# Kernel tuning notes

Hardware: AMD Instinct MI355X
Metric: run time of the kernel (lower is better)

## Reference

```python
import jax, jax.numpy as jnp
import numpy as np

N_NODE = 100000
N_EDGE = 800000
IN_DIM = 128
OUT_DIM = 128
ATTN_DIM = 64
N_REL = 200
N_ENT = 40000
BATCH = 64
N_RELA_ROWS = 2 * N_REL + 1  # 401


def setup_inputs() -> dict:
    key = jax.random.key(0)
    ks = jax.random.split(key, 16)
    # edges: [E, 6] -> col0: r_idx (batch idx), col2: rel, col4: sub, col5: obj
    r_idx = jax.random.randint(ks[0], (N_EDGE,), 0, BATCH)
    rel = jax.random.randint(ks[1], (N_EDGE,), 0, N_RELA_ROWS)
    sub = jax.random.randint(ks[2], (N_EDGE,), 0, N_NODE)
    obj = jax.random.randint(ks[3], (N_EDGE,), 0, N_NODE)
    zeros_col = jnp.zeros((N_EDGE,), dtype=jnp.int32)
    edges = jnp.stack([r_idx, zeros_col, rel, zeros_col, sub, obj], axis=1)

    hidden = jax.random.normal(ks[4], (N_NODE, IN_DIM), dtype=jnp.float32)
    q_sub = jax.random.randint(ks[5], (BATCH,), 0, N_ENT)
    q_rel = jax.random.randint(ks[6], (BATCH,), 0, N_RELA_ROWS)
    nodes = jnp.stack([
        jax.random.randint(ks[7], (N_NODE,), 0, BATCH),
        jax.random.randint(ks[8], (N_NODE,), 0, N_ENT)], axis=1)
    old_nodes_new_idx = jax.random.randint(ks[9], (50000,), 0, N_NODE)

    s = 0.05
    rela_embed = jax.random.normal(ks[10], (N_RELA_ROWS, IN_DIM), dtype=jnp.float32) * s
    Ws = jax.random.normal(ks[11], (IN_DIM, ATTN_DIM), dtype=jnp.float32) * s
    Wr = jax.random.normal(ks[12], (IN_DIM, ATTN_DIM), dtype=jnp.float32) * s
    Wqr = jax.random.normal(ks[13], (IN_DIM, ATTN_DIM), dtype=jnp.float32) * s
    bqr = jnp.zeros((ATTN_DIM,), dtype=jnp.float32)
    wa = jax.random.normal(ks[14], (ATTN_DIM, 1), dtype=jnp.float32) * s
    ba = jnp.zeros((1,), dtype=jnp.float32)
    W_h = jax.random.normal(ks[15], (IN_DIM, OUT_DIM), dtype=jnp.float32) * s

    return {"q_sub": q_sub, "q_rel": q_rel, "hidden": hidden, "edges": edges,
            "nodes": nodes, "old_nodes_new_idx": old_nodes_new_idx, "batchsize": BATCH,
            "rela_embed": rela_embed, "Ws": Ws, "Wr": Wr, "Wqr": Wqr, "bqr": bqr,
            "wa": wa, "ba": ba, "W_h": W_h}


def reference(q_sub, q_rel, hidden, edges, nodes, old_nodes_new_idx, batchsize,
              rela_embed, Ws, Wr, Wqr, bqr, wa, ba, W_h):
    sub = edges[:, 4]
    rel = edges[:, 2]
    obj = edges[:, 5]
    r_idx = edges[:, 0]
    n_node = nodes.shape[0]

    hs = hidden[sub]                    # [E, in_dim]  gather
    hr = rela_embed[rel]                # [E, in_dim]
    h_qr = rela_embed[q_rel][r_idx]     # [E, in_dim]

    # MESS_FUNC == 'TransE'
    message = hs + hr

    # attention MLP: sigmoid(w_alpha(relu(Ws hs + Wr hr + Wqr h_qr + bqr)))
    attn = jax.nn.relu(hs @ Ws + hr @ Wr + h_qr @ Wqr + bqr)  # [E, attn_dim]
    alpha = jax.nn.sigmoid(attn @ wa + ba)                     # [E, 1]
    message = alpha * message

    # AGG_FUNC == 'max': scatter-max into node buckets, empty buckets -> 0
    agg = jax.ops.segment_max(message, obj, num_segments=n_node)
    agg = jnp.where(jnp.isneginf(agg), 0.0, agg)

    # COMB_FUNC == 'discard', act is identity
    hidden_new = agg @ W_h              # [n_node, out_dim]
    return hidden_new
```

## Files before the change

kernel.cpp:

```cpp
#include <hip/hip_runtime.h>

#define N_NODE 100000
#define N_EDGE 800000
#define IN_DIM 128
#define OUT_DIM 128
#define ATTN 64
#define N_RELA 401
#define BATCH 64
#define CAP 64

#define SW_BLOCKS 3125
#define RELQ_BLOCKS 117
#define CNT_BLOCKS 3125

__device__ __forceinline__ unsigned short f2bf(float f) {
    unsigned u = __float_as_uint(f);
    u += 0x7FFFu + ((u >> 16) & 1u);
    return (unsigned short)(u >> 16);
}
__device__ __forceinline__ float bf2f(unsigned short u) {
    return __uint_as_float((unsigned)u << 16);
}

__global__ __launch_bounds__(256) void k_prep(
    const float* __restrict__ hidden, const float* __restrict__ Ws,
    unsigned short* __restrict__ sW_bf, unsigned* __restrict__ hid_bf,
    const float* __restrict__ rela, const float* __restrict__ Wr,
    const float* __restrict__ Wqr, const float* __restrict__ bqr,
    const int* __restrict__ q_rel, unsigned short* __restrict__ rW_bf,
    unsigned short* __restrict__ qW_bf, unsigned* __restrict__ rel_bf,
    const int* __restrict__ edges, int* __restrict__ cnt,
    unsigned* __restrict__ rec) {
    const int b = blockIdx.x;
    if (b < SW_BLOCKS) {
        __shared__ float h[4][8][IN_DIM];
        const int wv = threadIdx.x >> 6;
        const int t = threadIdx.x & 63;
        const long base = ((long)b * 4 + wv) * 8;
        const float4* hp = (const float4*)(hidden + base * IN_DIM);
        float4* hl = (float4*)(&h[wv][0][0]);
#pragma unroll
        for (int i = 0; i < 4; ++i) hl[i * 64 + t] = hp[i * 64 + t];
        __syncthreads();
        float acc[8] = {0.f, 0.f, 0.f, 0.f, 0.f, 0.f, 0.f, 0.f};
        for (int kq = 0; kq < IN_DIM / 4; ++kq) {
            const float w0 = Ws[(4 * kq + 0) * ATTN + t];
            const float w1 = Ws[(4 * kq + 1) * ATTN + t];
            const float w2 = Ws[(4 * kq + 2) * ATTN + t];
            const float w3 = Ws[(4 * kq + 3) * ATTN + t];
#pragma unroll
            for (int j = 0; j < 8; ++j) {
                float4 av = *(const float4*)(&h[wv][j][4 * kq]);
                acc[j] = fmaf(av.x, w0, acc[j]);
                acc[j] = fmaf(av.y, w1, acc[j]);
                acc[j] = fmaf(av.z, w2, acc[j]);
                acc[j] = fmaf(av.w, w3, acc[j]);
            }
        }
#pragma unroll
        for (int j = 0; j < 8; ++j) {
            sW_bf[(base + j) * ATTN + t] = f2bf(acc[j]);
            const float lo = h[wv][j][2 * t];
            const float hi = h[wv][j][2 * t + 1];
            hid_bf[(base + j) * 64 + t] =
                (unsigned)f2bf(lo) | ((unsigned)f2bf(hi) << 16);
        }
    } else if (b < SW_BLOCKS + RELQ_BLOCKS) {
        const int wv = threadIdx.x >> 6;
        const int t = threadIdx.x & 63;
        const int row = (b - SW_BLOCKS) * 4 + wv;
        if (row >= N_RELA + BATCH) return;
        if (row < N_RELA) {
            const float* hrow = rela + (long)row * IN_DIM;
            float acc = 0.f;
            for (int k = 0; k < IN_DIM; ++k) acc = fmaf(hrow[k], Wr[k * ATTN + t], acc);
            rW_bf[row * ATTN + t] = f2bf(acc);
            rel_bf[row * 64 + t] = (unsigned)f2bf(hrow[2 * t]) |
                                   ((unsigned)f2bf(hrow[2 * t + 1]) << 16);
        } else {
            const int q = row - N_RELA;
            const float* hrow = rela + (long)q_rel[q] * IN_DIM;
            float acc = bqr[t];
            for (int k = 0; k < IN_DIM; ++k) acc = fmaf(hrow[k], Wqr[k * ATTN + t], acc);
            qW_bf[q * ATTN + t] = f2bf(acc);
        }
    } else {
        const int e = (b - SW_BLOCKS - RELQ_BLOCKS) * 256 + threadIdx.x;
        if (e >= N_EDGE) return;
        const int* ed = edges + (long)e * 6;
        const int2 p0 = *(const int2*)(ed);
        const int2 p1 = *(const int2*)(ed + 2);
        const int2 p2 = *(const int2*)(ed + 4);
        const unsigned pk =
            ((unsigned)p2.x << 15) | ((unsigned)p1.x << 6) | (unsigned)p0.x;
        const int slot = atomicAdd(&cnt[p2.y], 1);
        if (slot < CAP) rec[(unsigned)p2.y * CAP + slot] = pk;
    }
}

__global__ __launch_bounds__(512) void k_fused(const unsigned* __restrict__ rec,
                                               const int* __restrict__ cnt,
                                               const unsigned* __restrict__ hid_bf,
                                               const unsigned* __restrict__ rel_bf,
                                               const unsigned short* __restrict__ sW_bf,
                                               const unsigned short* __restrict__ rW_bf,
                                               const unsigned short* __restrict__ qW_bf,
                                               const float* __restrict__ wa,
                                               const float* __restrict__ ba,
                                               const float* __restrict__ W_h,
                                               float* __restrict__ out) {
    __shared__ float a[8][IN_DIM];
    const int wv = threadIdx.x >> 6;
    const int lane = threadIdx.x & 63;
    const int l16 = lane & 15;
    const int grp = lane >> 4;
    const unsigned node = (unsigned)blockIdx.x * 8 + wv;
    const int deg = min(cnt[node], CAP);
    const float4 wav = ((const float4*)wa)[l16];
    const float bav = ba[0];
    const ushort4* sW4 = (const ushort4*)sW_bf;
    const ushort4* rW4 = (const ushort4*)rW_bf;
    const ushort4* qW4 = (const ushort4*)qW_bf;
    float m0 = -INFINITY, m1 = -INFINITY;

    if (deg > 0) {
        const unsigned myrec = rec[node * CAP + (unsigned)min(lane, deg - 1)];
        for (int i = 0; i < deg; i += 4) {
            const int gi = min(i + grp, deg - 1);
            const unsigned rg = __shfl(myrec, gi);
            const ushort4 s4 = sW4[(rg >> 15) * 16u + (unsigned)l16];
            const ushort4 r4 = rW4[((rg >> 6) & 511u) * 16u + (unsigned)l16];
            const ushort4 q4 = qW4[(rg & 63u) * 16u + (unsigned)l16];
            const int e1 = min(i + 1, deg - 1), e2 = min(i + 2, deg - 1),
                      e3 = min(i + 3, deg - 1);
            const unsigned rr0 = __shfl(myrec, i);
            const unsigned rr1 = __shfl(myrec, e1);
            const unsigned rr2 = __shfl(myrec, e2);
            const unsigned rr3 = __shfl(myrec, e3);
            const unsigned hs0 = hid_bf[(rr0 >> 15) * 64u + (unsigned)lane];
            const unsigned hs1 = hid_bf[(rr1 >> 15) * 64u + (unsigned)lane];
            const unsigned hs2 = hid_bf[(rr2 >> 15) * 64u + (unsigned)lane];
            const unsigned hs3 = hid_bf[(rr3 >> 15) * 64u + (unsigned)lane];
            const unsigned hr0 = rel_bf[((rr0 >> 6) & 511u) * 64u + (unsigned)lane];
            const unsigned hr1 = rel_bf[((rr1 >> 6) & 511u) * 64u + (unsigned)lane];
            const unsigned hr2 = rel_bf[((rr2 >> 6) & 511u) * 64u + (unsigned)lane];
            const unsigned hr3 = rel_bf[((rr3 >> 6) & 511u) * 64u + (unsigned)lane];
            float p = fmaxf(bf2f(s4.x) + bf2f(r4.x) + bf2f(q4.x), 0.f) * wav.x;
            p = fmaf(fmaxf(bf2f(s4.y) + bf2f(r4.y) + bf2f(q4.y), 0.f), wav.y, p);
            p = fmaf(fmaxf(bf2f(s4.z) + bf2f(r4.z) + bf2f(q4.z), 0.f), wav.z, p);
            p = fmaf(fmaxf(bf2f(s4.w) + bf2f(r4.w) + bf2f(q4.w), 0.f), wav.w, p);
            p += __shfl_xor(p, 1);
            p += __shfl_xor(p, 2);
            p += __shfl_xor(p, 4);
            p += __shfl_xor(p, 8);
            const float al_own = 1.f / (1.f + __expf(-(p + bav)));
            const float al0 = __shfl(al_own, 0);
            const float al1 = __shfl(al_own, 16);
            const float al2 = __shfl(al_own, 32);
            const float al3 = __shfl(al_own, 48);
            const int nb = deg - i;
            m0 = fmaxf(m0, al0 * (__uint_as_float(hs0 << 16) +
                                  __uint_as_float(hr0 << 16)));
            m1 = fmaxf(m1, al0 * (__uint_as_float(hs0 & 0xFFFF0000u) +
                                  __uint_as_float(hr0 & 0xFFFF0000u)));
            if (nb > 1) {
                m0 = fmaxf(m0, al1 * (__uint_as_float(hs1 << 16) +
                                      __uint_as_float(hr1 << 16)));
                m1 = fmaxf(m1, al1 * (__uint_as_float(hs1 & 0xFFFF0000u) +
                                      __uint_as_float(hr1 & 0xFFFF0000u)));
            }
            if (nb > 2) {
                m0 = fmaxf(m0, al2 * (__uint_as_float(hs2 << 16) +
                                      __uint_as_float(hr2 << 16)));
                m1 = fmaxf(m1, al2 * (__uint_as_float(hs2 & 0xFFFF0000u) +
                                      __uint_as_float(hr2 & 0xFFFF0000u)));
            }
            if (nb > 3) {
                m0 = fmaxf(m0, al3 * (__uint_as_float(hs3 << 16) +
                                      __uint_as_float(hr3 << 16)));
                m1 = fmaxf(m1, al3 * (__uint_as_float(hs3 & 0xFFFF0000u) +
                                      __uint_as_float(hr3 & 0xFFFF0000u)));
            }
        }
    } else {
        m0 = 0.f;
        m1 = 0.f;
    }
    a[wv][2 * lane] = m0;
    a[wv][2 * lane + 1] = m1;
    __syncthreads();
    const int c = threadIdx.x & 127;
    const int g = threadIdx.x >> 7;
    float acc0 = 0.f, acc1 = 0.f;
#pragma unroll 4
    for (int kq = 0; kq < IN_DIM / 4; ++kq) {
        const float4 a0 = *(const float4*)(&a[g][4 * kq]);
        const float4 a1 = *(const float4*)(&a[g + 4][4 * kq]);
        const float w0 = W_h[(4 * kq + 0) * OUT_DIM + c];
        const float w1 = W_h[(4 * kq + 1) * OUT_DIM + c];
        const float w2 = W_h[(4 * kq + 2) * OUT_DIM + c];
        const float w3 = W_h[(4 * kq + 3) * OUT_DIM + c];
        acc0 = fmaf(a0.x, w0, fmaf(a0.y, w1, fmaf(a0.z, w2, fmaf(a0.w, w3, acc0))));
        acc1 = fmaf(a1.x, w0, fmaf(a1.y, w1, fmaf(a1.z, w2, fmaf(a1.w, w3, acc1))));
    }
    const long nb2 = (long)blockIdx.x * 8;
    out[(nb2 + g) * OUT_DIM + c] = acc0;
    out[(nb2 + g + 4) * OUT_DIM + c] = acc1;
}

extern "C" void kernel_launch(void* const* d_in, const int* in_sizes, int n_in,
                              void* d_out, int out_size, void* d_ws, size_t ws_size,
                              hipStream_t stream) {
    const int* q_rel = (const int*)d_in[1];
    const float* hidden = (const float*)d_in[2];
    const int* edges = (const int*)d_in[3];
    const float* rela = (const float*)d_in[7];
    const float* Ws = (const float*)d_in[8];
    const float* Wr = (const float*)d_in[9];
    const float* Wqr = (const float*)d_in[10];
    const float* bqr = (const float*)d_in[11];
    const float* wa = (const float*)d_in[12];
    const float* ba = (const float*)d_in[13];
    const float* W_h = (const float*)d_in[14];
    float* out = (float*)d_out;

    char* ws = (char*)d_ws;
    unsigned short* sW_bf = (unsigned short*)(ws);
    unsigned* hid_bf = (unsigned*)(ws + 12800000);
    unsigned* rel_bf = (unsigned*)(ws + 38400000);
    unsigned short* rW_bf = (unsigned short*)(ws + 38502656);
    unsigned short* qW_bf = (unsigned short*)(ws + 38553984);
    int* cnt = (int*)(ws + 38562176);
    unsigned* rec = (unsigned*)(ws + 38962176);

    hipMemsetAsync(cnt, 0, N_NODE * sizeof(int), stream);
    hipLaunchKernelGGL(k_prep, dim3(SW_BLOCKS + RELQ_BLOCKS + CNT_BLOCKS), dim3(256),
                       0, stream, hidden, Ws, sW_bf, hid_bf, rela, Wr, Wqr, bqr,
                       q_rel, rW_bf, qW_bf, rel_bf, edges, cnt, rec);
    hipLaunchKernelGGL(k_fused, dim3(N_NODE / 8), dim3(512), 0, stream,
                       rec, cnt, hid_bf, rel_bf, sW_bf, rW_bf, qW_bf, wa, ba, W_h,
                       out);
}
```

Baseline: 354.7 us.

## Split output projection into separate fp16 MFMA kernel with staged aggregate

Moves the final agg @ W_h projection out of the fused gather/max kernel. The fused kernel now writes the aggregated rows as packed fp16 to a workspace buffer, and a new kernel multiplies them by a transposed fp16 copy of W_h with 16x16x32 MFMA instructions. The transposed copy is built by extra blocks in the prep kernel. This replaces the per-node scalar FP32 FMA loop, its shared-memory staging and its block barrier with matrix-core work. In exchange it adds a global round trip of about 25 MB, one more kernel launch, and fp16 rounding of both the aggregate and the weights.

```diff
diff --git a/kernel.cpp b/kernel.cpp
--- a/kernel.cpp
+++ b/kernel.cpp
@@ -1,4 +1,5 @@
 #include <hip/hip_runtime.h>
+#include <hip/hip_fp16.h>
 
 #define N_NODE 100000
 #define N_EDGE 800000
@@ -12,6 +13,10 @@
 #define SW_BLOCKS 3125
 #define RELQ_BLOCKS 117
 #define CNT_BLOCKS 3125
+#define WH_BLOCKS 16
+
+typedef _Float16 half8 __attribute__((ext_vector_type(8)));
+typedef float f32x4 __attribute__((ext_vector_type(4)));
 
 __device__ __forceinline__ unsigned short f2bf(float f) {
     unsigned u = __float_as_uint(f);
@@ -20,6 +25,11 @@
 }
 __device__ __forceinline__ float bf2f(unsigned short u) {
     return __uint_as_float((unsigned)u << 16);
+}
+__device__ __forceinline__ unsigned pack_h2(float lo, float hi) {
+    const unsigned short a = __half_as_ushort(__float2half_rn(lo));
+    const unsigned short b = __half_as_ushort(__float2half_rn(hi));
+    return (unsigned)a | ((unsigned)b << 16);
 }
 
 __global__ __launch_bounds__(256) void k_prep(
@@ -30,7 +40,8 @@
     const int* __restrict__ q_rel, unsigned short* __restrict__ rW_bf,
     unsigned short* __restrict__ qW_bf, unsigned* __restrict__ rel_bf,
     const int* __restrict__ edges, int* __restrict__ cnt,
-    unsigned* __restrict__ rec) {
+    unsigned* __restrict__ rec, const float* __restrict__ W_h,
+    unsigned* __restrict__ W_hT_h) {
     const int b = blockIdx.x;
     if (b < SW_BLOCKS) {
         __shared__ float h[4][8][IN_DIM];
@@ -84,7 +95,7 @@
             for (int k = 0; k < IN_DIM; ++k) acc = fmaf(hrow[k], Wqr[k * ATTN + t], acc);
             qW_bf[q * ATTN + t] = f2bf(acc);
         }
-    } else {
+    } else if (b < SW_BLOCKS + RELQ_BLOCKS + CNT_BLOCKS) {
         const int e = (b - SW_BLOCKS - RELQ_BLOCKS) * 256 + threadIdx.x;
         if (e >= N_EDGE) return;
         const int* ed = edges + (long)e * 6;
@@ -95,6 +106,17 @@
             ((unsigned)p2.x << 15) | ((unsigned)p1.x << 6) | (unsigned)p0.x;
         const int slot = atomicAdd(&cnt[p2.y], 1);
         if (slot < CAP) rec[(unsigned)p2.y * CAP + slot] = pk;
+    } else {
+        const int t0 = (b - SW_BLOCKS - RELQ_BLOCKS - CNT_BLOCKS) * 256 + threadIdx.x;
+#pragma unroll
+        for (int i = 0; i < 2; ++i) {
+            const int d = t0 * 2 + i;
+            const int c = d >> 6;
+            const int dd = d & 63;
+            const float lo = W_h[(2 * dd) * OUT_DIM + c];
+            const float hi = W_h[(2 * dd + 1) * OUT_DIM + c];
+            W_hT_h[d] = pack_h2(lo, hi);
+        }
     }
 }
 
@@ -107,11 +129,9 @@
                                                const unsigned short* __restrict__ qW_bf,
                                                const float* __restrict__ wa,
                                                const float* __restrict__ ba,
-                                               const float* __restrict__ W_h,
-                                               float* __restrict__ out) {
-    __shared__ float a[8][IN_DIM];
+                                               unsigned* __restrict__ agg_h) {
+    const int lane = threadIdx.x & 63;
     const int wv = threadIdx.x >> 6;
-    const int lane = threadIdx.x & 63;
     const int l16 = lane & 15;
     const int grp = lane >> 4;
     const unsigned node = (unsigned)blockIdx.x * 8 + wv;
@@ -186,26 +206,35 @@
         m0 = 0.f;
         m1 = 0.f;
     }
-    a[wv][2 * lane] = m0;
-    a[wv][2 * lane + 1] = m1;
-    __syncthreads();
-    const int c = threadIdx.x & 127;
-    const int g = threadIdx.x >> 7;
-    float acc0 = 0.f, acc1 = 0.f;
-#pragma unroll 4
-    for (int kq = 0; kq < IN_DIM / 4; ++kq) {
-        const float4 a0 = *(const float4*)(&a[g][4 * kq]);
-        const float4 a1 = *(const float4*)(&a[g + 4][4 * kq]);
-        const float w0 = W_h[(4 * kq + 0) * OUT_DIM + c];
-        const float w1 = W_h[(4 * kq + 1) * OUT_DIM + c];
-        const float w2 = W_h[(4 * kq + 2) * OUT_DIM + c];
-        const float w3 = W_h[(4 * kq + 3) * OUT_DIM + c];
-        acc0 = fmaf(a0.x, w0, fmaf(a0.y, w1, fmaf(a0.z, w2, fmaf(a0.w, w3, acc0))));
-        acc1 = fmaf(a1.x, w0, fmaf(a1.y, w1, fmaf(a1.z, w2, fmaf(a1.w, w3, acc1))));
+    agg_h[node * 64u + (unsigned)lane] = pack_h2(m0, m1);
+}
+
+__global__ __launch_bounds__(128) void k_out(const unsigned* __restrict__ agg_h,
+                                             const unsigned* __restrict__ W_hT_h,
+                                             float* __restrict__ out) {
+    const int wv = threadIdx.x >> 6;
+    const int lane = threadIdx.x & 63;
+    const int l15 = lane & 15;
+    const int lh = lane >> 4;
+    const int rb = (blockIdx.x * 2 + wv) * 16;
+    const unsigned* AU = agg_h + (unsigned)(rb + l15) * 64u + (unsigned)(lh * 4);
+    half8 af[4];
+#pragma unroll
+    for (int kk = 0; kk < 4; ++kk) af[kk] = *(const half8*)(AU + kk * 16);
+#pragma unroll
+    for (int n = 0; n < 8; ++n) {
+        const unsigned* BU = W_hT_h + (unsigned)(n * 16 + l15) * 64u + (unsigned)(lh * 4);
+        f32x4 acc = {0.f, 0.f, 0.f, 0.f};
+#pragma unroll
+        for (int kk = 0; kk < 4; ++kk)
+            acc = __builtin_amdgcn_mfma_f32_16x16x32_f16(
+                af[kk], *(const half8*)(BU + kk * 16), acc, 0, 0, 0);
+        float* op = out + (long)(rb + lh * 4) * OUT_DIM + n * 16 + l15;
+        op[0] = acc[0];
+        op[OUT_DIM] = acc[1];
+        op[2 * OUT_DIM] = acc[2];
+        op[3 * OUT_DIM] = acc[3];
     }
-    const long nb2 = (long)blockIdx.x * 8;
-    out[(nb2 + g) * OUT_DIM + c] = acc0;
-    out[(nb2 + g + 4) * OUT_DIM + c] = acc1;
 }
 
 extern "C" void kernel_launch(void* const* d_in, const int* in_sizes, int n_in,
@@ -232,12 +261,18 @@
     unsigned short* qW_bf = (unsigned short*)(ws + 38553984);
     int* cnt = (int*)(ws + 38562176);
     unsigned* rec = (unsigned*)(ws + 38962176);
+    unsigned* agg_h = (unsigned*)(ws + 64562176);
+    unsigned* W_hT_h = (unsigned*)(ws + 90162176);
 
     hipMemsetAsync(cnt, 0, N_NODE * sizeof(int), stream);
-    hipLaunchKernelGGL(k_prep, dim3(SW_BLOCKS + RELQ_BLOCKS + CNT_BLOCKS), dim3(256),
-                       0, stream, hidden, Ws, sW_bf, hid_bf, rela, Wr, Wqr, bqr,
-                       q_rel, rW_bf, qW_bf, rel_bf, edges, cnt, rec);
+    hipLaunchKernelGGL(k_prep,
+                       dim3(SW_BLOCKS + RELQ_BLOCKS + CNT_BLOCKS + WH_BLOCKS),
+                       dim3(256), 0, stream, hidden, Ws, sW_bf, hid_bf, rela, Wr,
+                       Wqr, bqr, q_rel, rW_bf, qW_bf, rel_bf, edges, cnt, rec,
+                       W_h, W_hT_h);
     hipLaunchKernelGGL(k_fused, dim3(N_NODE / 8), dim3(512), 0, stream,
-                       rec, cnt, hid_bf, rel_bf, sW_bf, rW_bf, qW_bf, wa, ba, W_h,
-                       out);
-}
+                       rec, cnt, hid_bf, rel_bf, sW_bf, rW_bf, qW_bf, wa, ba,
+                       agg_h);
+    hipLaunchKernelGGL(k_out, dim3(3125), dim3(128), 0, stream,
+                       agg_h, W_hT_h, out);
+}
```

After: 304.1 us. -14.3%, faster.
